# Kernel tuning notes

Measured on AMD Instinct MI355X. Metric: run time of the kernel, lower is better.

Reference implementation:

```python
import jax, jax.numpy as jnp
import numpy as np
import math

D_MODEL = 1024
D_STATE = 128
D_CONV = 4
D_INNER = 2048  # expand * d_model
DT_RANK = 64    # ceil(d_model / 16)
DT_MIN = 1e-3
DT_MAX = 0.1
BATCH = 2
SEQ = 2048


def setup_inputs() -> dict:
    key = jax.random.key(0)
    ks = jax.random.split(key, 8)
    x = jax.random.normal(ks[0], (BATCH, SEQ, D_MODEL), jnp.float32)
    W_in = jax.random.normal(ks[1], (2 * D_INNER, D_MODEL), jnp.float32) / math.sqrt(D_MODEL)
    W_out = jax.random.normal(ks[2], (D_MODEL, D_INNER), jnp.float32) / math.sqrt(D_INNER)
    conv_w = jax.random.normal(ks[3], (D_INNER, 1, D_CONV), jnp.float32) / math.sqrt(D_CONV)
    conv_b = jnp.zeros((D_INNER,), jnp.float32)
    W_x = jax.random.normal(ks[4], (DT_RANK + 2 * D_STATE, D_INNER), jnp.float32) / math.sqrt(D_INNER)
    dt_std = DT_RANK ** (-0.5) * DT_MAX
    W_dt = jax.random.uniform(ks[5], (D_INNER, DT_RANK), jnp.float32, -dt_std, dt_std)
    dt = jnp.exp(jax.random.uniform(ks[6], (D_INNER,), jnp.float32)
                 * (math.log(DT_MAX) - math.log(DT_MIN)) + math.log(DT_MIN))
    dt = jnp.clip(dt, DT_MIN, None)
    b_dt = dt + jnp.log(-jnp.expm1(-dt))  # inverse softplus init
    A_log = jnp.log(jnp.tile(jnp.arange(1, D_STATE + 1, dtype=jnp.float32), (D_INNER, 1)))
    Dp = jnp.ones((D_INNER,), jnp.float32)
    return {"x": x, "W_in": W_in, "W_out": W_out, "conv_w": conv_w, "conv_b": conv_b,
            "W_x": W_x, "W_dt": W_dt, "b_dt": b_dt, "A_log": A_log, "Dp": Dp}


def _silu(v):
    return v * jax.nn.sigmoid(v)


def _forward(x, W_in, W_out, conv_w, conv_b, W_x, W_dt, b_dt, A_log, Dp):
    bsz, seqlen, _ = x.shape
    xz = x @ W_in.T                              # (B, L, 2*D_INNER)
    xc, z = jnp.split(xz, 2, axis=-1)
    # causal depthwise conv1d (torch pads d_conv-1 both sides then truncates to L)
    xc_t = xc.transpose(0, 2, 1)                 # (B, D_INNER, L)
    conv = jax.lax.conv_general_dilated(
        xc_t, conv_w, window_strides=(1,), padding=[(D_CONV - 1, 0)],
        feature_group_count=D_INNER, dimension_numbers=('NCH', 'OIH', 'NCH'))
    u = _silu((conv + conv_b[None, :, None]).transpose(0, 2, 1))  # (B, L, D_INNER)

    # selective scan
    x_dbl = u @ W_x.T                            # (B, L, DT_RANK + 2*D_STATE)
    dt_lo = x_dbl[..., :DT_RANK]
    Bm = x_dbl[..., DT_RANK:DT_RANK + D_STATE]   # (B, L, N)
    Cm = x_dbl[..., DT_RANK + D_STATE:]          # (B, L, N)
    # NOTE: faithful to original, which adds dt_proj.bias twice
    dt = jax.nn.softplus(dt_lo @ W_dt.T + 2.0 * b_dt)  # (B, L, D_INNER)
    A = -jnp.exp(A_log)                          # (D_INNER, N)

    def step(h, inp):
        dt_t, B_t, C_t, u_t = inp                # (B,D),(B,N),(B,N),(B,D)
        dA = jnp.exp(dt_t[:, :, None] * A[None])            # (B, D, N)
        h = dA * h + (dt_t * u_t)[:, :, None] * B_t[:, None, :]
        y = jnp.einsum('bdn,bn->bd', h, C_t)
        return h, y

    h0 = jnp.zeros((bsz, D_INNER, D_STATE), u.dtype)
    _, ys = jax.lax.scan(step, h0, (dt.transpose(1, 0, 2), Bm.transpose(1, 0, 2),
                                    Cm.transpose(1, 0, 2), u.transpose(1, 0, 2)))
    y = ys.transpose(1, 0, 2) + u * Dp           # (B, L, D_INNER)
    y = y * _silu(z)
    return y @ W_out.T                           # (B, L, D_MODEL)


def reference(x, W_in, W_out, conv_w, conv_b, W_x, W_dt, b_dt, A_log, Dp):
    return _forward(x, W_in, W_out, conv_w, conv_b, W_x, W_dt, b_dt, A_log, Dp)
```

## Files before the change

kernel.cpp:

```cpp
#include <hip/hip_runtime.h>
#include <stdint.h>
#include <math.h>

#define D_MODEL 1024
#define D_STATE 128
#define D_INNER 2048
#define DT_RANK 64
#define BATCH   2
#define SEQ     2048
#define TOKENS  (BATCH*SEQ)
#define NPROJ   (DT_RANK + 2*D_STATE)

typedef unsigned short u16;
typedef __attribute__((ext_vector_type(4))) float f32x4;
typedef __attribute__((ext_vector_type(8))) short s16x8;
typedef __attribute__((ext_vector_type(4))) unsigned short u16x4;

#if __has_builtin(__builtin_amdgcn_exp2f)
#define EXP2(x) __builtin_amdgcn_exp2f(x)
#else
#define EXP2(x) __expf((x) * 0.6931471805599453f)
#endif

static __device__ __forceinline__ u16 f2bf(float f) {
  unsigned u = __builtin_bit_cast(unsigned, f);
  return (u16)((u + 0x7FFFu + ((u >> 16) & 1u)) >> 16);
}
static __device__ __forceinline__ float bf2f(u16 h) {
  return __builtin_bit_cast(float, ((unsigned)h) << 16);
}

static __device__ __forceinline__ void gload_lds16(const void* g, void* l) {
  __builtin_amdgcn_global_load_lds(
      (const __attribute__((address_space(1))) void*)g,
      (__attribute__((address_space(3))) void*)l, 16, 0, 0);
}

__global__ void k_cvt_bf16(const float* __restrict__ in, u16* __restrict__ out, int n4) {
  int i = blockIdx.x * blockDim.x + threadIdx.x;
  if (i >= n4) return;
  f32x4 v = ((const f32x4*)in)[i];
  u16x4 o;
  o.x = f2bf(v.x); o.y = f2bf(v.y); o.z = f2bf(v.z); o.w = f2bf(v.w);
  ((u16x4*)out)[i] = o;
}

#define BM 128
#define BN 128
#define BK 64

template<int EPI>
__global__ __launch_bounds__(256) void k_gemm_bt(
    const u16* __restrict__ A, const u16* __restrict__ B,
    void* __restrict__ C, const float* __restrict__ bias,
    const u16* __restrict__ U,
    int M, int N, int K, int ldc)
{
  __shared__ __align__(16) u16 As[BM*BK];
  __shared__ __align__(16) u16 Bs[BN*BK];
  const int tid  = threadIdx.x;
  const int lane = tid & 63;
  const int wid  = tid >> 6;
  const int wr   = (wid >> 1) * 64;
  const int wc   = (wid & 1) * 64;
  const int bm   = blockIdx.x * BM;
  const int bn   = blockIdx.y * BN;
  const int lr   = lane & 15;
  const int lk   = (lane >> 4) * 8;

  f32x4 acc[4][4] = {};

  for (int k0 = 0; k0 < K; k0 += BK) {
    #pragma unroll
    for (int i = 0; i < 4; ++i) {
      int c   = tid + i * 256;
      int row = c >> 3;
      int col = (c & 7) * 8;
      const u16* ga = A + (size_t)(bm + row) * K + (k0 + col);
      gload_lds16(ga, As + (size_t)c * 8);
      int brow = bn + row; brow = brow < N ? brow : N - 1;
      const u16* gb = B + (size_t)brow * K + (k0 + col);
      gload_lds16(gb, Bs + (size_t)c * 8);
    }
    __syncthreads();

    #pragma unroll
    for (int kk = 0; kk < BK; kk += 32) {
      s16x8 af[4], bf[4];
      #pragma unroll
      for (int m = 0; m < 4; ++m)
        af[m] = *(const s16x8*)(As + (size_t)(wr + m*16 + lr) * BK + kk + lk);
      #pragma unroll
      for (int n = 0; n < 4; ++n)
        bf[n] = *(const s16x8*)(Bs + (size_t)(wc + n*16 + lr) * BK + kk + lk);
      #pragma unroll
      for (int m = 0; m < 4; ++m)
        #pragma unroll
        for (int n = 0; n < 4; ++n)
          acc[m][n] = __builtin_amdgcn_mfma_f32_16x16x32_bf16(af[m], bf[n], acc[m][n], 0, 0, 0);
    }
    __syncthreads();
  }

  const int orow0 = bm + wr + (lane >> 4) * 4;
  const int ocol0 = bn + wc + lr;
  #pragma unroll
  for (int m = 0; m < 4; ++m) {
    #pragma unroll
    for (int n = 0; n < 4; ++n) {
      int col = ocol0 + n * 16;
      if (col >= N) continue;
      #pragma unroll
      for (int r = 0; r < 4; ++r) {
        int row = orow0 + m * 16 + r;
        float v = acc[m][n][r];
        if (EPI == 3) {
          v = v + 2.0f * bias[col];
          v = (v > 20.0f) ? v : log1pf(__expf(v));
          float uu = bf2f(U[(size_t)row * D_INNER + col]);
          ((float2*)C)[(size_t)row * ldc + col] = make_float2(v, v * uu);
        } else if (EPI == 1) {
          ((u16*)C)[(size_t)row * ldc + col] = f2bf(v);
        } else {
          ((float*)C)[(size_t)row * ldc + col] = v;
        }
      }
    }
  }
}

__global__ __launch_bounds__(256) void k_conv_silu(
    const u16* __restrict__ xz, const float* __restrict__ cw,
    const float* __restrict__ cb, u16* __restrict__ u)
{
  int idx = blockIdx.x * 256 + threadIdx.x;
  int d   = idx & (D_INNER - 1);
  int tok = idx >> 11;
  int t   = tok & (SEQ - 1);
  int b   = tok >> 11;
  f32x4 w = *(const f32x4*)(cw + (size_t)d * 4);
  float acc = cb[d];
  #pragma unroll
  for (int j = 0; j < 4; ++j) {
    int tt = t - 3 + j;
    if (tt >= 0)
      acc += bf2f(xz[(size_t)(b * SEQ + tt) * (2*D_INNER) + d]) * w[j];
  }
  float s = acc / (1.0f + __expf(-acc));
  u[(size_t)tok * D_INNER + d] = f2bf(s);
}

__global__ void k_split(const float* __restrict__ xdbl, u16* __restrict__ dtlo,
                        float* __restrict__ BC)
{
  int idx = blockIdx.x * 256 + threadIdx.x;
  if (idx >= TOKENS * NPROJ) return;
  int row = idx / NPROJ;
  int c   = idx - row * NPROJ;
  float v = xdbl[idx];
  if (c < DT_RANK) {
    dtlo[(size_t)row * DT_RANK + c] = f2bf(v);
  } else if (c < DT_RANK + D_STATE) {
    int n = c - DT_RANK;
    BC[(size_t)row * 256 + (n >> 1) * 4 + (n & 1)] = v;
  } else {
    int n = c - DT_RANK - D_STATE;
    BC[(size_t)row * 256 + (n >> 1) * 4 + 2 + (n & 1)] = v;
  }
}

#define SCHUNK 32

__global__ __launch_bounds__(256) void k_scan(
    const float2* __restrict__ dtdu, const float* __restrict__ BC,
    const float* __restrict__ A_log, u16* __restrict__ ysT)
{
  __shared__ float red[4][SCHUNK * 64];
  const int lane = threadIdx.x & 63;
  const int wid  = threadIdx.x >> 6;
  int gw = __builtin_amdgcn_readfirstlane(blockIdx.x * 4 + wid);
  const int b = gw >> 11;
  const int d = gw & (D_INNER - 1);

  float2 al = *(const float2*)(A_log + (size_t)d * D_STATE + 2 * lane);
  const float A0 = -__expf(al.x) * 1.44269504f;
  const float A1 = -__expf(al.y) * 1.44269504f;
  float h0 = 0.f, h1 = 0.f;

  const float2* dcol = dtdu + (size_t)b * SEQ * D_INNER + d;
  const float*  BCb  = BC + (size_t)b * SEQ * 256 + 4 * lane;
  u16* yo = ysT + ((size_t)d * BATCH + b) * SEQ;

  float* myred = red[wid];
  float* wptr[8];
  #pragma unroll
  for (int j = 0; j < 8; ++j) wptr[j] = myred + (lane ^ (j << 2));

  const int r  = lane & 31;
  const int hf = lane >> 5;
  const float* rrow = myred + r * 64;

  for (int t0 = 0; t0 < SEQ; t0 += SCHUNK) {
    #pragma unroll
    for (int tt = 0; tt < SCHUNK; ++tt) {
      float2 sd = dcol[(size_t)(t0 + tt) * D_INNER];
      f32x4 bc = *(const f32x4*)(BCb + (size_t)(t0 + tt) * 256);
      float dA0 = EXP2(sd.x * A0);
      float dA1 = EXP2(sd.x * A1);
      h0 = fmaf(dA0, h0, sd.y * bc.x);
      h1 = fmaf(dA1, h1, sd.y * bc.y);
      float yp = fmaf(h1, bc.w, h0 * bc.z);
      wptr[tt & 7][tt * 64] = yp;
    }
    __syncthreads();
    f32x4 s4 = {0.f, 0.f, 0.f, 0.f};
    #pragma unroll
    for (int k = 0; k < 8; ++k) {
      int off = (hf * 32 + k * 4) ^ ((r & 7) << 2);
      s4 += *(const f32x4*)(rrow + off);
    }
    float s = (s4.x + s4.y) + (s4.z + s4.w);
    float y = s + __shfl_xor(s, 32);
    if (hf == 0) yo[t0 + r] = f2bf(y);
    __syncthreads();
  }
}

__global__ __launch_bounds__(256) void k_gate(
    const u16* __restrict__ ysT, const u16* __restrict__ ub,
    const u16* __restrict__ xz, const float* __restrict__ Dp,
    u16* __restrict__ yg)
{
  __shared__ u16 tile[64][68];
  const int tid  = threadIdx.x;
  const int c    = tid & 63;
  const int rb   = tid >> 6;
  const int tok0 = blockIdx.x * 64;
  const int d0   = blockIdx.y * 64;
  const int bb   = tok0 >> 11;
  const int t0   = tok0 & (SEQ - 1);

  #pragma unroll
  for (int j = 0; j < 16; ++j) {
    int dl = rb + j * 4;
    tile[dl][c] = ysT[((size_t)(d0 + dl) * BATCH + bb) * SEQ + t0 + c];
  }
  __syncthreads();
  #pragma unroll
  for (int j = 0; j < 16; ++j) {
    int tl  = rb + j * 4;
    int tok = tok0 + tl;
    int dd  = d0 + c;
    float y = bf2f(tile[c][tl]);
    float uu = bf2f(ub[(size_t)tok * D_INNER + dd]);
    float z  = bf2f(xz[(size_t)tok * (2*D_INNER) + D_INNER + dd]);
    float v  = (y + uu * Dp[dd]) * (z / (1.0f + __expf(-z)));
    yg[(size_t)tok * D_INNER + dd] = f2bf(v);
  }
}

extern "C" void kernel_launch(void* const* d_in, const int* in_sizes, int n_in,
                              void* d_out, int out_size, void* d_ws, size_t ws_size,
                              hipStream_t stream) {
  (void)in_sizes; (void)n_in; (void)out_size; (void)ws_size;
  const float* x      = (const float*)d_in[0];
  const float* W_in   = (const float*)d_in[1];
  const float* W_out  = (const float*)d_in[2];
  const float* conv_w = (const float*)d_in[3];
  const float* conv_b = (const float*)d_in[4];
  const float* W_x    = (const float*)d_in[5];
  const float* W_dt   = (const float*)d_in[6];
  const float* b_dt   = (const float*)d_in[7];
  const float* A_log  = (const float*)d_in[8];
  const float* Dp     = (const float*)d_in[9];

  size_t off = 0;
  char* wsb = (char*)d_ws;
  auto alloc = [&](size_t bytes) -> void* {
    void* p = wsb + off;
    off += (bytes + 255) & ~(size_t)255;
    return p;
  };
  u16*    x_bf    = (u16*)alloc((size_t)TOKENS * D_MODEL * 2);
  u16*    Win_bf  = (u16*)alloc((size_t)2 * D_INNER * D_MODEL * 2);
  u16*    Wx_bf   = (u16*)alloc((size_t)NPROJ * D_INNER * 2);
  u16*    Wdt_bf  = (u16*)alloc((size_t)D_INNER * DT_RANK * 2);
  u16*    Wout_bf = (u16*)alloc((size_t)D_MODEL * D_INNER * 2);
  u16*    xz_bf   = (u16*)alloc((size_t)TOKENS * 2 * D_INNER * 2);
  u16*    u_bf    = (u16*)alloc((size_t)TOKENS * D_INNER * 2);
  float*  xdbl    = (float*)alloc((size_t)TOKENS * NPROJ * 4);
  u16*    dtlo_bf = (u16*)alloc((size_t)TOKENS * DT_RANK * 2);
  float*  BC_f    = (float*)alloc((size_t)TOKENS * 256 * 4);
  float2* dtdu    = (float2*)alloc((size_t)TOKENS * D_INNER * 8);
  u16*    ysT     = (u16*)alloc((size_t)D_INNER * TOKENS * 2);
  u16*    yg      = (u16*)alloc((size_t)TOKENS * D_INNER * 2);

  auto cvt = [&](const float* src, u16* dst, size_t n) {
    int n4 = (int)(n / 4);
    k_cvt_bf16<<<(n4 + 255) / 256, 256, 0, stream>>>(src, dst, n4);
  };
  cvt(x,     x_bf,    (size_t)TOKENS * D_MODEL);
  cvt(W_in,  Win_bf,  (size_t)2 * D_INNER * D_MODEL);
  cvt(W_x,   Wx_bf,   (size_t)NPROJ * D_INNER);
  cvt(W_dt,  Wdt_bf,  (size_t)D_INNER * DT_RANK);
  cvt(W_out, Wout_bf, (size_t)D_MODEL * D_INNER);

  dim3 blk(256);
  k_gemm_bt<1><<<dim3(TOKENS/128, (2*D_INNER)/128), blk, 0, stream>>>(
      x_bf, Win_bf, xz_bf, nullptr, nullptr, TOKENS, 2*D_INNER, D_MODEL, 2*D_INNER);
  k_conv_silu<<<(TOKENS * D_INNER) / 256, blk, 0, stream>>>(xz_bf, conv_w, conv_b, u_bf);
  k_gemm_bt<0><<<dim3(TOKENS/128, (NPROJ + 127)/128), blk, 0, stream>>>(
      u_bf, Wx_bf, xdbl, nullptr, nullptr, TOKENS, NPROJ, D_INNER, NPROJ);
  k_split<<<((TOKENS * NPROJ) + 255) / 256, blk, 0, stream>>>(xdbl, dtlo_bf, BC_f);
  k_gemm_bt<3><<<dim3(TOKENS/128, D_INNER/128), blk, 0, stream>>>(
      dtlo_bf, Wdt_bf, dtdu, b_dt, u_bf, TOKENS, D_INNER, DT_RANK, D_INNER);
  k_scan<<<(BATCH * D_INNER) / 4, blk, 0, stream>>>(dtdu, BC_f, A_log, ysT);
  k_gate<<<dim3(TOKENS/64, D_INNER/64), blk, 0, stream>>>(ysT, u_bf, xz_bf, Dp, yg);
  k_gemm_bt<0><<<dim3(TOKENS/128, D_MODEL/128), blk, 0, stream>>>(
      yg, Wout_bf, d_out, nullptr, nullptr, TOKENS, D_MODEL, D_INNER, D_MODEL);
}
```

Before: 537.8 us.

## Store dt/du channel-major for contiguous scan reads and drop scan barriers

The dt-projection GEMM epilogue now writes the (dt, dt*u) pairs transposed, channel-major, with log2(e) folded into dt. Each scan wave can then read a contiguous run of timesteps for its channel instead of a strided column. The scan's per-wave LDS reduction uses a padded row stride instead of an XOR swizzle, and the __syncthreads calls are removed because each wave only touches its own buffer. The price is that the GEMM epilogue's stores become strided across tokens, and launch bounds now request 4 blocks per CU.

Result: slower. 618.8 us (+15.1%).

```diff
diff --git a/kernel.cpp b/kernel.cpp
--- a/kernel.cpp
+++ b/kernel.cpp
@@ -21,6 +21,7 @@
 #else
 #define EXP2(x) __expf((x) * 0.6931471805599453f)
 #endif
+#define L2E 1.44269504088896f
 
 static __device__ __forceinline__ u16 f2bf(float f) {
   unsigned u = __builtin_bit_cast(unsigned, f);
@@ -118,7 +119,7 @@
           v = v + 2.0f * bias[col];
           v = (v > 20.0f) ? v : log1pf(__expf(v));
           float uu = bf2f(U[(size_t)row * D_INNER + col]);
-          ((float2*)C)[(size_t)row * ldc + col] = make_float2(v, v * uu);
+          ((float2*)C)[(size_t)col * TOKENS + row] = make_float2(v * L2E, v * uu);
         } else if (EPI == 1) {
           ((u16*)C)[(size_t)row * ldc + col] = f2bf(v);
         } else {
@@ -170,59 +171,57 @@
 }
 
 #define SCHUNK 32
-
-__global__ __launch_bounds__(256) void k_scan(
-    const float2* __restrict__ dtdu, const float* __restrict__ BC,
+#define RPAD 65
+
+__global__ __launch_bounds__(256, 4) void k_scan(
+    const float2* __restrict__ dtq, const float* __restrict__ BC,
     const float* __restrict__ A_log, u16* __restrict__ ysT)
 {
-  __shared__ float red[4][SCHUNK * 64];
+  __shared__ float red[4][SCHUNK * RPAD];
   const int lane = threadIdx.x & 63;
   const int wid  = threadIdx.x >> 6;
-  int gw = __builtin_amdgcn_readfirstlane(blockIdx.x * 4 + wid);
+  const int gw = blockIdx.x * 4 + wid;
   const int b = gw >> 11;
   const int d = gw & (D_INNER - 1);
 
   float2 al = *(const float2*)(A_log + (size_t)d * D_STATE + 2 * lane);
-  const float A0 = -__expf(al.x) * 1.44269504f;
-  const float A1 = -__expf(al.y) * 1.44269504f;
+  const float A0 = -__expf(al.x);
+  const float A1 = -__expf(al.y);
   float h0 = 0.f, h1 = 0.f;
 
-  const float2* dcol = dtdu + (size_t)b * SEQ * D_INNER + d;
-  const float*  BCb  = BC + (size_t)b * SEQ * 256 + 4 * lane;
+  const float2* dbase = dtq + (size_t)d * TOKENS + b * SEQ;
+  asm("" : "+v"(dbase));
+  const float* BCb = BC + (size_t)b * SEQ * 256 + 4 * lane;
   u16* yo = ysT + ((size_t)d * BATCH + b) * SEQ;
 
   float* myred = red[wid];
-  float* wptr[8];
-  #pragma unroll
-  for (int j = 0; j < 8; ++j) wptr[j] = myred + (lane ^ (j << 2));
-
   const int r  = lane & 31;
   const int hf = lane >> 5;
-  const float* rrow = myred + r * 64;
+  const float* rrow = myred + r * RPAD + hf * 32;
 
   for (int t0 = 0; t0 < SEQ; t0 += SCHUNK) {
     #pragma unroll
     for (int tt = 0; tt < SCHUNK; ++tt) {
-      float2 sd = dcol[(size_t)(t0 + tt) * D_INNER];
+      float2 sd = dbase[t0 + tt];
       f32x4 bc = *(const f32x4*)(BCb + (size_t)(t0 + tt) * 256);
       float dA0 = EXP2(sd.x * A0);
       float dA1 = EXP2(sd.x * A1);
       h0 = fmaf(dA0, h0, sd.y * bc.x);
       h1 = fmaf(dA1, h1, sd.y * bc.y);
       float yp = fmaf(h1, bc.w, h0 * bc.z);
-      wptr[tt & 7][tt * 64] = yp;
-    }
-    __syncthreads();
-    f32x4 s4 = {0.f, 0.f, 0.f, 0.f};
+      myred[tt * RPAD + lane] = yp;
+    }
+    float s0 = 0.f, s1 = 0.f, s2 = 0.f, s3 = 0.f;
     #pragma unroll
     for (int k = 0; k < 8; ++k) {
-      int off = (hf * 32 + k * 4) ^ ((r & 7) << 2);
-      s4 += *(const f32x4*)(rrow + off);
-    }
-    float s = (s4.x + s4.y) + (s4.z + s4.w);
+      s0 += rrow[k];
+      s1 += rrow[k + 8];
+      s2 += rrow[k + 16];
+      s3 += rrow[k + 24];
+    }
+    float s = (s0 + s1) + (s2 + s3);
     float y = s + __shfl_xor(s, 32);
     if (hf == 0) yo[t0 + r] = f2bf(y);
-    __syncthreads();
   }
 }
 
@@ -291,7 +290,7 @@
   float*  xdbl    = (float*)alloc((size_t)TOKENS * NPROJ * 4);
   u16*    dtlo_bf = (u16*)alloc((size_t)TOKENS * DT_RANK * 2);
   float*  BC_f    = (float*)alloc((size_t)TOKENS * 256 * 4);
-  float2* dtdu    = (float2*)alloc((size_t)TOKENS * D_INNER * 8);
+  float2* dtq     = (float2*)alloc((size_t)TOKENS * D_INNER * 8);
   u16*    ysT     = (u16*)alloc((size_t)D_INNER * TOKENS * 2);
   u16*    yg      = (u16*)alloc((size_t)TOKENS * D_INNER * 2);
 
@@ -313,8 +312,8 @@
       u_bf, Wx_bf, xdbl, nullptr, nullptr, TOKENS, NPROJ, D_INNER, NPROJ);
   k_split<<<((TOKENS * NPROJ) + 255) / 256, blk, 0, stream>>>(xdbl, dtlo_bf, BC_f);
   k_gemm_bt<3><<<dim3(TOKENS/128, D_INNER/128), blk, 0, stream>>>(
-      dtlo_bf, Wdt_bf, dtdu, b_dt, u_bf, TOKENS, D_INNER, DT_RANK, D_INNER);
-  k_scan<<<(BATCH * D_INNER) / 4, blk, 0, stream>>>(dtdu, BC_f, A_log, ysT);
+      dtlo_bf, Wdt_bf, dtq, b_dt, u_bf, TOKENS, D_INNER, DT_RANK, 0);
+  k_scan<<<(BATCH * D_INNER) / 4, blk, 0, stream>>>(dtq, BC_f, A_log, ysT);
   k_gate<<<dim3(TOKENS/64, D_INNER/64), blk, 0, stream>>>(ysT, u_bf, xz_bf, Dp, yg);
   k_gemm_bt<0><<<dim3(TOKENS/128, D_MODEL/128), blk, 0, stream>>>(
       yg, Wout_bf, d_out, nullptr, nullptr, TOKENS, D_MODEL, D_INNER, D_MODEL);
```
